# Performance work log

Hardware: AMD Instinct MI355X
Metric: run time of the kernel (lower is better)

## Reference

```python
import jax, jax.numpy as jnp
import numpy as np

N_NODES = 500_000
N_EDGES = 16_000_000


def setup_inputs() -> dict:
    key = jax.random.key(0)
    ks = jax.random.split(key, 8)
    x = jax.random.normal(ks[0], (N_NODES, 6), dtype=jnp.float32)
    edge_index = jax.random.randint(ks[1], (2, N_EDGES), 0, N_NODES, dtype=jnp.int64)
    conv_w = jax.random.normal(ks[2], (4, 6), dtype=jnp.float32) * 0.4
    conv_b = jax.random.normal(ks[3], (4,), dtype=jnp.float32) * 0.1
    fc1_w = jax.random.normal(ks[4], (64, 4), dtype=jnp.float32) * 0.5
    fc1_b = jax.random.normal(ks[5], (64,), dtype=jnp.float32) * 0.1
    fc3_w = jax.random.normal(ks[6], (10, 64), dtype=jnp.float32) * 0.125
    fc3_b = jax.random.normal(ks[7], (10,), dtype=jnp.float32) * 0.1
    return {"x": x, "edge_index": edge_index, "conv_w": conv_w, "conv_b": conv_b,
            "fc1_w": fc1_w, "fc1_b": fc1_b, "fc3_w": fc3_w, "fc3_b": fc3_b}


def reference(x, edge_index, conv_w, conv_b, fc1_w, fc1_b, fc3_w, fc3_b):
    n = x.shape[0]
    loop = jnp.arange(n, dtype=edge_index.dtype)
    # PyG GCNConv default: add self-loops, symmetric normalization
    row = jnp.concatenate([edge_index[0], loop])  # source
    col = jnp.concatenate([edge_index[1], loop])  # target (aggregation index)
    deg = jax.ops.segment_sum(jnp.ones_like(col, dtype=x.dtype), col, num_segments=n)
    dinv = jnp.where(deg > 0, deg ** -0.5, 0.0).astype(x.dtype)
    norm = dinv[row] * dinv[col]                  # [E+N]
    h = x @ conv_w.T                              # [N, 4]
    msg = h[row] * norm[:, None]                  # gather + scale
    agg = jax.ops.segment_sum(msg, col, num_segments=n) + conv_b  # scatter-add
    t = jnp.tanh(agg)
    # F.dropout treated as identity (deterministic eval reference)
    g = jnp.mean(t, axis=0, keepdims=True)        # global_mean_pool, batch=None -> [1, 4]
    hdn = jax.nn.relu(g @ fc1_w.T + fc1_b)
    out = hdn @ fc3_w.T + fc3_b                   # [1, output_size]
    return out
```

## Files before the change

kernel.cpp:

```cpp
#include <hip/hip_runtime.h>
#include <hip/hip_fp16.h>
#include <math.h>


constexpr int NP = 1024;
constexpr int SHIFT = 10;
constexpr unsigned MASK = 1023;
constexpr int NPART_MAX = 512;
constexpr int EPB = 8192;
constexpr int BINB = 512;
constexpr int BT = 512;

struct alignas(8) Half4 { __half2 a, b; };


__global__ __launch_bounds__(BINB) void k_bin(const int* __restrict__ row,
                                              const int* __restrict__ col, int E,
                                              int P, int cap, int* __restrict__ cursor,
                                              unsigned* __restrict__ binned) {
    __shared__ unsigned lbuf[EPB];
    __shared__ int lcount[NPART_MAX];
    __shared__ int lbase[NPART_MAX];
    __shared__ int gbase[NPART_MAX];
    __shared__ int lpos[NPART_MAX];
    __shared__ int sc[NPART_MAX];

    int t = threadIdx.x;
    int start = blockIdx.x * EPB;
    int end = min(start + EPB, E);
    bool full = (end - start) == EPB;

    lcount[t] = 0; lpos[t] = 0;
    __syncthreads();

    if (full) {
        const int4* c4 = (const int4*)(col + start);
#pragma unroll
        for (int i = 0; i < EPB / 4 / BINB; ++i) {
            int4 c = c4[t + i * BINB];
            atomicAdd(&lcount[c.x >> SHIFT], 1);
            atomicAdd(&lcount[c.y >> SHIFT], 1);
            atomicAdd(&lcount[c.z >> SHIFT], 1);
            atomicAdd(&lcount[c.w >> SHIFT], 1);
        }
    } else {
        for (int e = start + t; e < end; e += BINB)
            atomicAdd(&lcount[col[e] >> SHIFT], 1);
    }
    __syncthreads();

    sc[t] = lcount[t];
    __syncthreads();
    for (int off = 1; off < NPART_MAX; off <<= 1) {
        int v = (t >= off) ? sc[t - off] : 0;
        __syncthreads();
        sc[t] += v;
        __syncthreads();
    }
    lbase[t] = sc[t] - lcount[t];
    if (t < P) {
        int c = lcount[t];
        gbase[t] = (c > 0) ? atomicAdd(&cursor[t], c) : 0;
    }
    __syncthreads();

    if (full) {
        const int4* c4 = (const int4*)(col + start);
        const int4* r4 = (const int4*)(row + start);
#pragma unroll
        for (int i = 0; i < EPB / 4 / BINB; ++i) {
            int4 c = c4[t + i * BINB];
            int4 r = r4[t + i * BINB];
            int part, slot;
            part = c.x >> SHIFT; slot = atomicAdd(&lpos[part], 1);
            lbuf[lbase[part] + slot] = ((unsigned)r.x << SHIFT) | ((unsigned)c.x & MASK);
            part = c.y >> SHIFT; slot = atomicAdd(&lpos[part], 1);
            lbuf[lbase[part] + slot] = ((unsigned)r.y << SHIFT) | ((unsigned)c.y & MASK);
            part = c.z >> SHIFT; slot = atomicAdd(&lpos[part], 1);
            lbuf[lbase[part] + slot] = ((unsigned)r.z << SHIFT) | ((unsigned)c.z & MASK);
            part = c.w >> SHIFT; slot = atomicAdd(&lpos[part], 1);
            lbuf[lbase[part] + slot] = ((unsigned)r.w << SHIFT) | ((unsigned)c.w & MASK);
        }
    } else {
        for (int e = start + t; e < end; e += BINB) {
            int r = row[e], c = col[e];
            int part = c >> SHIFT;
            int slot = atomicAdd(&lpos[part], 1);
            lbuf[lbase[part] + slot] = ((unsigned)r << SHIFT) | ((unsigned)c & MASK);
        }
    }
    __syncthreads();

    int lane = t & 63;
    int wave = t >> 6;
    const int nwaves = BINB / 64;
    for (int part = wave; part < P; part += nwaves) {
        int cnt = lcount[part];
        if (cnt == 0) continue;
        int lb = lbase[part];
        int gb = gbase[part];
        unsigned* dst = binned + (size_t)part * cap;
        for (int j = lane; j < cnt; j += 64) {
            int slot = gb + j;
            if (slot < cap) dst[slot] = lbuf[lb + j];
        }
    }
}

__global__ __launch_bounds__(BT) void k_part_node(const unsigned* __restrict__ binned,
                                                  const int* __restrict__ cursor, int cap,
                                                  const float* __restrict__ x,
                                                  const float* __restrict__ conv_w, int n,
                                                  Half4* __restrict__ ph,
                                                  float* __restrict__ dinvg) {
    __shared__ int degs[NP];
    __shared__ float w[24];
    int part = blockIdx.x;
    int tid = threadIdx.x;
    if (tid < 24) w[tid] = conv_w[tid];
    for (int i = tid; i < NP; i += BT) degs[i] = 0;
    __syncthreads();
    int cnt = min(cursor[part], cap);
    const unsigned* bin = binned + (size_t)part * cap;
    const uint4* bin4 = (const uint4*)bin;
    int cnt4 = cnt >> 2;
    for (int i = tid; i < cnt4; i += BT) {
        uint4 v = bin4[i];
        atomicAdd(&degs[v.x & MASK], 1);
        atomicAdd(&degs[v.y & MASK], 1);
        atomicAdd(&degs[v.z & MASK], 1);
        atomicAdd(&degs[v.w & MASK], 1);
    }
    for (int e = (cnt4 << 2) + tid; e < cnt; e += BT)
        atomicAdd(&degs[bin[e] & MASK], 1);
    __syncthreads();
    int base = part * NP;
    for (int i = tid; i < NP; i += BT) {
        int node = base + i;
        if (node >= n) continue;
        float dinv = rsqrtf((float)(degs[i] + 1));
        const float* xr = x + (size_t)node * 6;
        float2 a = *(const float2*)xr;
        float2 b = *(const float2*)(xr + 2);
        float2 cc = *(const float2*)(xr + 4);
        float xv[6] = {a.x, a.y, b.x, b.y, cc.x, cc.y};
        float h0 = 0.f, h1 = 0.f, h2 = 0.f, h3 = 0.f;
#pragma unroll
        for (int j = 0; j < 6; ++j) {
            h0 += xv[j] * w[j];
            h1 += xv[j] * w[6 + j];
            h2 += xv[j] * w[12 + j];
            h3 += xv[j] * w[18 + j];
        }
        Half4 o;
        o.a = __floats2half2_rn(h0 * dinv, h1 * dinv);
        o.b = __floats2half2_rn(h2 * dinv, h3 * dinv);
        ph[node] = o;
        dinvg[node] = dinv;
    }
}

__global__ __launch_bounds__(BT) void k_acc(const unsigned* __restrict__ binned,
                                            const int* __restrict__ cursor, int cap,
                                            const Half4* __restrict__ ph,
                                            const float* __restrict__ dinvg,
                                            const float* __restrict__ conv_b, int n,
                                            float* __restrict__ gsum) {
    __shared__ float S[NP * 5];
    __shared__ float4 red[BT / 64];
    int part = blockIdx.x;
    int tid = threadIdx.x;
    for (int i = tid; i < NP * 5; i += BT) S[i] = 0.f;
    __syncthreads();
    int cnt = min(cursor[part], cap);
    const unsigned* bin = binned + (size_t)part * cap;
    const uint4* bin4 = (const uint4*)bin;
    int cnt4 = cnt >> 2;
    for (int i = tid; i < cnt4; i += BT) {
        uint4 v = bin4[i];
        Half4 h0 = ph[v.x >> SHIFT];
        Half4 h1 = ph[v.y >> SHIFT];
        Half4 h2 = ph[v.z >> SHIFT];
        Half4 h3 = ph[v.w >> SHIFT];
        float2 a, b; float* s;
        a = __half22float2(h0.a); b = __half22float2(h0.b); s = &S[(v.x & MASK) * 5];
        atomicAdd(s + 0, a.x); atomicAdd(s + 1, a.y); atomicAdd(s + 2, b.x); atomicAdd(s + 3, b.y);
        a = __half22float2(h1.a); b = __half22float2(h1.b); s = &S[(v.y & MASK) * 5];
        atomicAdd(s + 0, a.x); atomicAdd(s + 1, a.y); atomicAdd(s + 2, b.x); atomicAdd(s + 3, b.y);
        a = __half22float2(h2.a); b = __half22float2(h2.b); s = &S[(v.z & MASK) * 5];
        atomicAdd(s + 0, a.x); atomicAdd(s + 1, a.y); atomicAdd(s + 2, b.x); atomicAdd(s + 3, b.y);
        a = __half22float2(h3.a); b = __half22float2(h3.b); s = &S[(v.w & MASK) * 5];
        atomicAdd(s + 0, a.x); atomicAdd(s + 1, a.y); atomicAdd(s + 2, b.x); atomicAdd(s + 3, b.y);
    }
    for (int e = (cnt4 << 2) + tid; e < cnt; e += BT) {
        unsigned v = bin[e];
        Half4 h = ph[v >> SHIFT];
        float2 a = __half22float2(h.a), b = __half22float2(h.b);
        float* s = &S[(v & MASK) * 5];
        atomicAdd(s + 0, a.x); atomicAdd(s + 1, a.y); atomicAdd(s + 2, b.x); atomicAdd(s + 3, b.y);
    }
    __syncthreads();
    float b0 = conv_b[0], b1 = conv_b[1], b2 = conv_b[2], b3 = conv_b[3];
    float4 acc = {0.f, 0.f, 0.f, 0.f};
    int base = part * NP;
    for (int i = tid; i < NP; i += BT) {
        int node = base + i;
        if (node >= n) continue;
        float di = dinvg[node];
        Half4 hp = ph[node];
        float2 pa = __half22float2(hp.a), pb = __half22float2(hp.b);
        acc.x += tanhf(di * (S[i * 5 + 0] + pa.x) + b0);
        acc.y += tanhf(di * (S[i * 5 + 1] + pa.y) + b1);
        acc.z += tanhf(di * (S[i * 5 + 2] + pb.x) + b2);
        acc.w += tanhf(di * (S[i * 5 + 3] + pb.y) + b3);
    }
#pragma unroll
    for (int off = 32; off > 0; off >>= 1) {
        acc.x += __shfl_down(acc.x, off);
        acc.y += __shfl_down(acc.y, off);
        acc.z += __shfl_down(acc.z, off);
        acc.w += __shfl_down(acc.w, off);
    }
    int lane = tid & 63, wv = tid >> 6;
    if (lane == 0) red[wv] = acc;
    __syncthreads();
    if (tid == 0) {
        float4 tt = red[0];
        for (int k = 1; k < BT / 64; ++k) {
            tt.x += red[k].x; tt.y += red[k].y; tt.z += red[k].z; tt.w += red[k].w;
        }
        unsafeAtomicAdd(&gsum[0], tt.x);
        unsafeAtomicAdd(&gsum[1], tt.y);
        unsafeAtomicAdd(&gsum[2], tt.z);
        unsafeAtomicAdd(&gsum[3], tt.w);
    }
}

__global__ void k_head(const float* __restrict__ gsum,
                       const float* __restrict__ fc1w, const float* __restrict__ fc1b,
                       const float* __restrict__ fc3w, const float* __restrict__ fc3b,
                       float* __restrict__ out, int n) {
    __shared__ float hdn[64];
    int t = threadIdx.x;
    float g[4];
    float inv_n = 1.0f / (float)n;
#pragma unroll
    for (int j = 0; j < 4; ++j) g[j] = gsum[j] * inv_n;
    if (t < 64) {
        float a = fc1b[t];
#pragma unroll
        for (int j = 0; j < 4; ++j) a += g[j] * fc1w[t * 4 + j];
        hdn[t] = fmaxf(a, 0.f);
    }
    __syncthreads();
    if (t < 10) {
        float a = fc3b[t];
#pragma unroll
        for (int k = 0; k < 64; ++k) a += hdn[k] * fc3w[t * 64 + k];
        out[t] = a;
    }
}


__global__ void k_deg(const int* __restrict__ col, int n_edges, int* __restrict__ deg) {
    int t = blockIdx.x * blockDim.x + threadIdx.x;
    int base = t * 4;
    if (base + 4 <= n_edges) {
        int4 c = *(const int4*)(col + base);
        atomicAdd(&deg[c.x], 1); atomicAdd(&deg[c.y], 1);
        atomicAdd(&deg[c.z], 1); atomicAdd(&deg[c.w], 1);
    } else {
        for (int e = base; e < n_edges; ++e) atomicAdd(&deg[col[e]], 1);
    }
}

__global__ void k_node(const float* __restrict__ x, const float* __restrict__ conv_w,
                       const int* __restrict__ deg, float4* __restrict__ p, int n) {
    int i = blockIdx.x * blockDim.x + threadIdx.x;
    if (i >= n) return;
    const float* xr = x + (size_t)i * 6;
    float2 a = *(const float2*)xr;
    float2 b = *(const float2*)(xr + 2);
    float2 c = *(const float2*)(xr + 4);
    float xv[6] = {a.x, a.y, b.x, b.y, c.x, c.y};
    float dinv = rsqrtf((float)(deg[i] + 1));
    float h0 = 0.f, h1 = 0.f, h2 = 0.f, h3 = 0.f;
#pragma unroll
    for (int j = 0; j < 6; ++j) {
        h0 += xv[j] * conv_w[j];
        h1 += xv[j] * conv_w[6 + j];
        h2 += xv[j] * conv_w[12 + j];
        h3 += xv[j] * conv_w[18 + j];
    }
    float4 o; o.x = h0 * dinv; o.y = h1 * dinv; o.z = h2 * dinv; o.w = h3 * dinv;
    p[i] = o;
}

__global__ void k_scatter(const int* __restrict__ row, const int* __restrict__ col, int n_edges,
                          const float4* __restrict__ p, float* __restrict__ S) {
    int t = blockIdx.x * blockDim.x + threadIdx.x;
    int base = t * 2;
    if (base + 2 <= n_edges) {
        int2 r = *(const int2*)(row + base);
        int2 c = *(const int2*)(col + base);
        float4 p0 = p[r.x], p1 = p[r.y];
        float* s0 = S + 4 * c.x;
        unsafeAtomicAdd(s0 + 0, p0.x); unsafeAtomicAdd(s0 + 1, p0.y);
        unsafeAtomicAdd(s0 + 2, p0.z); unsafeAtomicAdd(s0 + 3, p0.w);
        float* s1 = S + 4 * c.y;
        unsafeAtomicAdd(s1 + 0, p1.x); unsafeAtomicAdd(s1 + 1, p1.y);
        unsafeAtomicAdd(s1 + 2, p1.z); unsafeAtomicAdd(s1 + 3, p1.w);
    } else {
        for (int e = base; e < n_edges; ++e) {
            int r = row[e], c = col[e];
            float4 pv = p[r];
            float* s = S + 4 * c;
            unsafeAtomicAdd(s + 0, pv.x); unsafeAtomicAdd(s + 1, pv.y);
            unsafeAtomicAdd(s + 2, pv.z); unsafeAtomicAdd(s + 3, pv.w);
        }
    }
}

__global__ void k_reduce(const float4* __restrict__ S4, const float4* __restrict__ p,
                         const int* __restrict__ deg, const float* __restrict__ conv_b,
                         int n, float* __restrict__ gsum) {
    int i = blockIdx.x * blockDim.x + threadIdx.x;
    float4 v = {0.f, 0.f, 0.f, 0.f};
    if (i < n) {
        float dinv = rsqrtf((float)(deg[i] + 1));
        float4 s = S4[i];
        float4 pp = p[i];
        v.x = tanhf(dinv * (s.x + pp.x) + conv_b[0]);
        v.y = tanhf(dinv * (s.y + pp.y) + conv_b[1]);
        v.z = tanhf(dinv * (s.z + pp.z) + conv_b[2]);
        v.w = tanhf(dinv * (s.w + pp.w) + conv_b[3]);
    }
#pragma unroll
    for (int off = 32; off > 0; off >>= 1) {
        v.x += __shfl_down(v.x, off);
        v.y += __shfl_down(v.y, off);
        v.z += __shfl_down(v.z, off);
        v.w += __shfl_down(v.w, off);
    }
    __shared__ float4 lds[4];
    int lane = threadIdx.x & 63, w = threadIdx.x >> 6;
    if (lane == 0) lds[w] = v;
    __syncthreads();
    if (threadIdx.x == 0) {
        float4 tt = lds[0];
        for (int k = 1; k < 4; ++k) {
            tt.x += lds[k].x; tt.y += lds[k].y; tt.z += lds[k].z; tt.w += lds[k].w;
        }
        unsafeAtomicAdd(&gsum[0], tt.x); unsafeAtomicAdd(&gsum[1], tt.y);
        unsafeAtomicAdd(&gsum[2], tt.z); unsafeAtomicAdd(&gsum[3], tt.w);
    }
}


extern "C" void kernel_launch(void* const* d_in, const int* in_sizes, int n_in,
                              void* d_out, int out_size, void* d_ws, size_t ws_size,
                              hipStream_t stream) {
    const float* x      = (const float*)d_in[0];
    const int*   ei     = (const int*)d_in[1];
    const float* conv_w = (const float*)d_in[2];
    const float* conv_b = (const float*)d_in[3];
    const float* fc1w   = (const float*)d_in[4];
    const float* fc1b   = (const float*)d_in[5];
    const float* fc3w   = (const float*)d_in[6];
    const float* fc3b   = (const float*)d_in[7];

    int n = in_sizes[0] / 6;
    int E = in_sizes[1] / 2;
    const int* row = ei;
    const int* col = ei + E;

    int P = (n + NP - 1) / NP;
    int avg = (E + P - 1) / P;
    int cap = ((avg + avg / 8 + 2048) + 15) & ~15;

    size_t off = 0;
    size_t cursor_off = off;          off += (size_t)P * sizeof(int);
    off = (off + 15) & ~(size_t)15;
    size_t gsum_off = off;            off += 4 * sizeof(float);
    size_t zero_end = off;
    off = (off + 15) & ~(size_t)15;
    size_t dinv_off = off;            off += (size_t)n * sizeof(float);
    off = (off + 15) & ~(size_t)15;
    size_t ph_off = off;              off += (size_t)n * sizeof(Half4);
    off = (off + 15) & ~(size_t)15;
    size_t bin_off = off;             off += (size_t)P * cap * sizeof(unsigned);
    size_t need = off;

    char* ws = (char*)d_ws;
    bool use_bin = (ws_size >= need) && (P <= NPART_MAX) && (n < (1 << 22));

    if (use_bin) {
        int* cursor = (int*)(ws + cursor_off);
        float* gsum = (float*)(ws + gsum_off);
        float* dinvg = (float*)(ws + dinv_off);
        Half4* ph = (Half4*)(ws + ph_off);
        unsigned* binned = (unsigned*)(ws + bin_off);

        hipMemsetAsync(d_ws, 0, zero_end, stream);
        int bin_blocks = (E + EPB - 1) / EPB;
        k_bin<<<bin_blocks, BINB, 0, stream>>>(row, col, E, P, cap, cursor, binned);
        k_part_node<<<P, BT, 0, stream>>>(binned, cursor, cap, x, conv_w, n, ph, dinvg);
        k_acc<<<P, BT, 0, stream>>>(binned, cursor, cap, ph, dinvg, conv_b, n, gsum);
        k_head<<<1, 64, 0, stream>>>(gsum, fc1w, fc1b, fc3w, fc3b, (float*)d_out, n);
    } else {
        size_t o = 0;
        int* deg = (int*)(ws + o);      o += (size_t)n * sizeof(int);
        o = (o + 15) & ~(size_t)15;
        float* S = (float*)(ws + o);    o += (size_t)n * 4 * sizeof(float);
        float* gsum = (float*)(ws + o);
        size_t zend = o + 4 * sizeof(float);
        o = (zend + 15) & ~(size_t)15;
        float4* p = (float4*)(ws + o);

        hipMemsetAsync(d_ws, 0, zend, stream);
        int t1 = (E + 3) / 4;
        k_deg<<<(t1 + 255) / 256, 256, 0, stream>>>(col, E, deg);
        k_node<<<(n + 255) / 256, 256, 0, stream>>>(x, conv_w, deg, p, n);
        int t3 = (E + 1) / 2;
        k_scatter<<<(t3 + 255) / 256, 256, 0, stream>>>(row, col, E, p, S);
        k_reduce<<<(n + 255) / 256, 256, 0, stream>>>((const float4*)S, p, deg, conv_b, n, gsum);
        k_head<<<1, 64, 0, stream>>>(gsum, fc1w, fc1b, fc3w, fc3b, (float*)d_out, n);
    }
}
```

Before: 624.3 us.

## Split per-partition degree and accumulate work across multiple blocks with global merge

Each partition's binned edges are now processed by SPLIT blocks instead of one. The per-partition degree pass and the accumulate pass each merge their shared-memory partials into global arrays with atomics. The node transform and the final tanh/mean reduction move into separate grid-wide kernels. Nontemporal loads and stores are used for streaming binned data and edge rows, and the bin capacity slack is reduced. This targets low occupancy from only about 489 blocks per pass, at the cost of extra kernels, global atomics, a larger memset, and a risk of bin overflow with the tighter cap.

```diff
diff --git a/kernel.cpp b/kernel.cpp
--- a/kernel.cpp
+++ b/kernel.cpp
@@ -10,8 +10,13 @@
 constexpr int EPB = 8192;
 constexpr int BINB = 512;
 constexpr int BT = 512;
+constexpr int SPLIT = 4;
 
 struct alignas(8) Half4 { __half2 a, b; };
+
+typedef unsigned u32x4 __attribute__((ext_vector_type(4)));
+typedef int      i32x4 __attribute__((ext_vector_type(4)));
+typedef float    f32x4 __attribute__((ext_vector_type(4)));
 
 
 __global__ __launch_bounds__(BINB) void k_bin(const int* __restrict__ row,
@@ -66,11 +71,11 @@
 
     if (full) {
         const int4* c4 = (const int4*)(col + start);
-        const int4* r4 = (const int4*)(row + start);
+        const i32x4* r4 = (const i32x4*)(row + start);
 #pragma unroll
         for (int i = 0; i < EPB / 4 / BINB; ++i) {
             int4 c = c4[t + i * BINB];
-            int4 r = r4[t + i * BINB];
+            i32x4 r = __builtin_nontemporal_load(&r4[t + i * BINB]);
             int part, slot;
             part = c.x >> SHIFT; slot = atomicAdd(&lpos[part], 1);
             lbuf[lbase[part] + slot] = ((unsigned)r.x << SHIFT) | ((unsigned)c.x & MASK);
@@ -102,82 +107,88 @@
         unsigned* dst = binned + (size_t)part * cap;
         for (int j = lane; j < cnt; j += 64) {
             int slot = gb + j;
-            if (slot < cap) dst[slot] = lbuf[lb + j];
-        }
-    }
-}
-
-__global__ __launch_bounds__(BT) void k_part_node(const unsigned* __restrict__ binned,
-                                                  const int* __restrict__ cursor, int cap,
-                                                  const float* __restrict__ x,
-                                                  const float* __restrict__ conv_w, int n,
-                                                  Half4* __restrict__ ph,
-                                                  float* __restrict__ dinvg) {
+            if (slot < cap) __builtin_nontemporal_store(lbuf[lb + j], &dst[slot]);
+        }
+    }
+}
+
+__global__ __launch_bounds__(BT) void k_deg_bin(const unsigned* __restrict__ binned,
+                                                const int* __restrict__ cursor, int cap,
+                                                int n, int* __restrict__ deg) {
     __shared__ int degs[NP];
-    __shared__ float w[24];
-    int part = blockIdx.x;
+    int part = blockIdx.x / SPLIT;
+    int sub = blockIdx.x - part * SPLIT;
     int tid = threadIdx.x;
-    if (tid < 24) w[tid] = conv_w[tid];
     for (int i = tid; i < NP; i += BT) degs[i] = 0;
     __syncthreads();
     int cnt = min(cursor[part], cap);
     const unsigned* bin = binned + (size_t)part * cap;
-    const uint4* bin4 = (const uint4*)bin;
+    const u32x4* bin4 = (const u32x4*)bin;
     int cnt4 = cnt >> 2;
-    for (int i = tid; i < cnt4; i += BT) {
-        uint4 v = bin4[i];
+    for (int i = tid + sub * BT; i < cnt4; i += BT * SPLIT) {
+        u32x4 v = __builtin_nontemporal_load(&bin4[i]);
         atomicAdd(&degs[v.x & MASK], 1);
         atomicAdd(&degs[v.y & MASK], 1);
         atomicAdd(&degs[v.z & MASK], 1);
         atomicAdd(&degs[v.w & MASK], 1);
     }
-    for (int e = (cnt4 << 2) + tid; e < cnt; e += BT)
-        atomicAdd(&degs[bin[e] & MASK], 1);
+    if (sub == 0) {
+        for (int e = (cnt4 << 2) + tid; e < cnt; e += BT)
+            atomicAdd(&degs[bin[e] & MASK], 1);
+    }
     __syncthreads();
     int base = part * NP;
     for (int i = tid; i < NP; i += BT) {
         int node = base + i;
-        if (node >= n) continue;
-        float dinv = rsqrtf((float)(degs[i] + 1));
-        const float* xr = x + (size_t)node * 6;
-        float2 a = *(const float2*)xr;
-        float2 b = *(const float2*)(xr + 2);
-        float2 cc = *(const float2*)(xr + 4);
-        float xv[6] = {a.x, a.y, b.x, b.y, cc.x, cc.y};
-        float h0 = 0.f, h1 = 0.f, h2 = 0.f, h3 = 0.f;
-#pragma unroll
-        for (int j = 0; j < 6; ++j) {
-            h0 += xv[j] * w[j];
-            h1 += xv[j] * w[6 + j];
-            h2 += xv[j] * w[12 + j];
-            h3 += xv[j] * w[18 + j];
-        }
-        Half4 o;
-        o.a = __floats2half2_rn(h0 * dinv, h1 * dinv);
-        o.b = __floats2half2_rn(h2 * dinv, h3 * dinv);
-        ph[node] = o;
-        dinvg[node] = dinv;
-    }
-}
-
-__global__ __launch_bounds__(BT) void k_acc(const unsigned* __restrict__ binned,
-                                            const int* __restrict__ cursor, int cap,
-                                            const Half4* __restrict__ ph,
-                                            const float* __restrict__ dinvg,
-                                            const float* __restrict__ conv_b, int n,
-                                            float* __restrict__ gsum) {
+        if (node < n && degs[i] > 0) atomicAdd(&deg[node], degs[i]);
+    }
+}
+
+__global__ __launch_bounds__(256) void k_node2(const float* __restrict__ x,
+                                               const float* __restrict__ conv_w,
+                                               const int* __restrict__ deg, int n,
+                                               Half4* __restrict__ ph) {
+    __shared__ float w[24];
+    if (threadIdx.x < 24) w[threadIdx.x] = conv_w[threadIdx.x];
+    __syncthreads();
+    int i = blockIdx.x * 256 + threadIdx.x;
+    if (i >= n) return;
+    float dinv = rsqrtf((float)(deg[i] + 1));
+    const float* xr = x + (size_t)i * 6;
+    float2 a = *(const float2*)xr;
+    float2 b = *(const float2*)(xr + 2);
+    float2 cc = *(const float2*)(xr + 4);
+    float xv[6] = {a.x, a.y, b.x, b.y, cc.x, cc.y};
+    float h0 = 0.f, h1 = 0.f, h2 = 0.f, h3 = 0.f;
+#pragma unroll
+    for (int j = 0; j < 6; ++j) {
+        h0 += xv[j] * w[j];
+        h1 += xv[j] * w[6 + j];
+        h2 += xv[j] * w[12 + j];
+        h3 += xv[j] * w[18 + j];
+    }
+    Half4 o;
+    o.a = __floats2half2_rn(h0 * dinv, h1 * dinv);
+    o.b = __floats2half2_rn(h2 * dinv, h3 * dinv);
+    ph[i] = o;
+}
+
+__global__ __launch_bounds__(BT) void k_acc2(const unsigned* __restrict__ binned,
+                                             const int* __restrict__ cursor, int cap,
+                                             const Half4* __restrict__ ph,
+                                             float* __restrict__ Sg) {
     __shared__ float S[NP * 5];
-    __shared__ float4 red[BT / 64];
-    int part = blockIdx.x;
+    int part = blockIdx.x / SPLIT;
+    int sub = blockIdx.x - part * SPLIT;
     int tid = threadIdx.x;
     for (int i = tid; i < NP * 5; i += BT) S[i] = 0.f;
     __syncthreads();
     int cnt = min(cursor[part], cap);
     const unsigned* bin = binned + (size_t)part * cap;
-    const uint4* bin4 = (const uint4*)bin;
+    const u32x4* bin4 = (const u32x4*)bin;
     int cnt4 = cnt >> 2;
-    for (int i = tid; i < cnt4; i += BT) {
-        uint4 v = bin4[i];
+    for (int i = tid + sub * BT; i < cnt4; i += BT * SPLIT) {
+        u32x4 v = __builtin_nontemporal_load(&bin4[i]);
         Half4 h0 = ph[v.x >> SHIFT];
         Half4 h1 = ph[v.y >> SHIFT];
         Half4 h2 = ph[v.z >> SHIFT];
@@ -192,41 +203,53 @@
         a = __half22float2(h3.a); b = __half22float2(h3.b); s = &S[(v.w & MASK) * 5];
         atomicAdd(s + 0, a.x); atomicAdd(s + 1, a.y); atomicAdd(s + 2, b.x); atomicAdd(s + 3, b.y);
     }
-    for (int e = (cnt4 << 2) + tid; e < cnt; e += BT) {
-        unsigned v = bin[e];
-        Half4 h = ph[v >> SHIFT];
-        float2 a = __half22float2(h.a), b = __half22float2(h.b);
-        float* s = &S[(v & MASK) * 5];
-        atomicAdd(s + 0, a.x); atomicAdd(s + 1, a.y); atomicAdd(s + 2, b.x); atomicAdd(s + 3, b.y);
-    }
-    __syncthreads();
-    float b0 = conv_b[0], b1 = conv_b[1], b2 = conv_b[2], b3 = conv_b[3];
-    float4 acc = {0.f, 0.f, 0.f, 0.f};
-    int base = part * NP;
-    for (int i = tid; i < NP; i += BT) {
-        int node = base + i;
-        if (node >= n) continue;
-        float di = dinvg[node];
-        Half4 hp = ph[node];
+    if (sub == 0) {
+        for (int e = (cnt4 << 2) + tid; e < cnt; e += BT) {
+            unsigned v = bin[e];
+            Half4 h = ph[v >> SHIFT];
+            float2 a = __half22float2(h.a), b = __half22float2(h.b);
+            float* s = &S[(v & MASK) * 5];
+            atomicAdd(s + 0, a.x); atomicAdd(s + 1, a.y); atomicAdd(s + 2, b.x); atomicAdd(s + 3, b.y);
+        }
+    }
+    __syncthreads();
+    float* dst = Sg + (size_t)part * NP * 4;
+    for (int i = tid; i < NP * 4; i += BT) {
+        unsafeAtomicAdd(&dst[i], S[(i >> 2) * 5 + (i & 3)]);
+    }
+}
+
+__global__ __launch_bounds__(256) void k_finish(const float* __restrict__ Sg,
+                                                const Half4* __restrict__ ph,
+                                                const int* __restrict__ deg,
+                                                const float* __restrict__ conv_b, int n,
+                                                float* __restrict__ gsum) {
+    int i = blockIdx.x * 256 + threadIdx.x;
+    float4 v = {0.f, 0.f, 0.f, 0.f};
+    if (i < n) {
+        float dinv = rsqrtf((float)(deg[i] + 1));
+        f32x4 s = __builtin_nontemporal_load((const f32x4*)Sg + i);
+        Half4 hp = ph[i];
         float2 pa = __half22float2(hp.a), pb = __half22float2(hp.b);
-        acc.x += tanhf(di * (S[i * 5 + 0] + pa.x) + b0);
-        acc.y += tanhf(di * (S[i * 5 + 1] + pa.y) + b1);
-        acc.z += tanhf(di * (S[i * 5 + 2] + pb.x) + b2);
-        acc.w += tanhf(di * (S[i * 5 + 3] + pb.y) + b3);
+        v.x = tanhf(dinv * (s.x + pa.x) + conv_b[0]);
+        v.y = tanhf(dinv * (s.y + pa.y) + conv_b[1]);
+        v.z = tanhf(dinv * (s.z + pb.x) + conv_b[2]);
+        v.w = tanhf(dinv * (s.w + pb.y) + conv_b[3]);
     }
 #pragma unroll
     for (int off = 32; off > 0; off >>= 1) {
-        acc.x += __shfl_down(acc.x, off);
-        acc.y += __shfl_down(acc.y, off);
-        acc.z += __shfl_down(acc.z, off);
-        acc.w += __shfl_down(acc.w, off);
-    }
-    int lane = tid & 63, wv = tid >> 6;
-    if (lane == 0) red[wv] = acc;
-    __syncthreads();
-    if (tid == 0) {
+        v.x += __shfl_down(v.x, off);
+        v.y += __shfl_down(v.y, off);
+        v.z += __shfl_down(v.z, off);
+        v.w += __shfl_down(v.w, off);
+    }
+    __shared__ float4 red[4];
+    int lane = threadIdx.x & 63, w = threadIdx.x >> 6;
+    if (lane == 0) red[w] = v;
+    __syncthreads();
+    if (threadIdx.x == 0) {
         float4 tt = red[0];
-        for (int k = 1; k < BT / 64; ++k) {
+        for (int k = 1; k < 4; ++k) {
             tt.x += red[k].x; tt.y += red[k].y; tt.z += red[k].z; tt.w += red[k].w;
         }
         unsafeAtomicAdd(&gsum[0], tt.x);
@@ -376,15 +399,17 @@
 
     int P = (n + NP - 1) / NP;
     int avg = (E + P - 1) / P;
-    int cap = ((avg + avg / 8 + 2048) + 15) & ~15;
+    int cap = ((avg + avg / 32 + 1024) + 15) & ~15;
 
     size_t off = 0;
     size_t cursor_off = off;          off += (size_t)P * sizeof(int);
     off = (off + 15) & ~(size_t)15;
     size_t gsum_off = off;            off += 4 * sizeof(float);
+    off = (off + 15) & ~(size_t)15;
+    size_t deg_off = off;             off += (size_t)n * sizeof(int);
+    off = (off + 15) & ~(size_t)15;
+    size_t S_off = off;               off += (size_t)P * NP * 4 * sizeof(float);
     size_t zero_end = off;
-    off = (off + 15) & ~(size_t)15;
-    size_t dinv_off = off;            off += (size_t)n * sizeof(float);
     off = (off + 15) & ~(size_t)15;
     size_t ph_off = off;              off += (size_t)n * sizeof(Half4);
     off = (off + 15) & ~(size_t)15;
@@ -397,15 +422,18 @@
     if (use_bin) {
         int* cursor = (int*)(ws + cursor_off);
         float* gsum = (float*)(ws + gsum_off);
-        float* dinvg = (float*)(ws + dinv_off);
+        int* deg = (int*)(ws + deg_off);
+        float* Sg = (float*)(ws + S_off);
         Half4* ph = (Half4*)(ws + ph_off);
         unsigned* binned = (unsigned*)(ws + bin_off);
 
         hipMemsetAsync(d_ws, 0, zero_end, stream);
         int bin_blocks = (E + EPB - 1) / EPB;
         k_bin<<<bin_blocks, BINB, 0, stream>>>(row, col, E, P, cap, cursor, binned);
-        k_part_node<<<P, BT, 0, stream>>>(binned, cursor, cap, x, conv_w, n, ph, dinvg);
-        k_acc<<<P, BT, 0, stream>>>(binned, cursor, cap, ph, dinvg, conv_b, n, gsum);
+        k_deg_bin<<<P * SPLIT, BT, 0, stream>>>(binned, cursor, cap, n, deg);
+        k_node2<<<(n + 255) / 256, 256, 0, stream>>>(x, conv_w, deg, n, ph);
+        k_acc2<<<P * SPLIT, BT, 0, stream>>>(binned, cursor, cap, ph, Sg);
+        k_finish<<<(n + 255) / 256, 256, 0, stream>>>(Sg, ph, deg, conv_b, n, gsum);
         k_head<<<1, 64, 0, stream>>>(gsum, fc1w, fc1b, fc3w, fc3b, (float*)d_out, n);
     } else {
         size_t o = 0;
```

Measured after the change: 751.2 us. +20.3%, slower.

## Split degree counting across blocks and add nontemporal loads/stores for bins

Applied to the files above, without the earlier changes.

Replaces the per-partition degree+node kernel with a degree kernel that splits each partition across SPLIT blocks and merges counts into a global degree array with atomics, then a separate flat node kernel computes dinv and the projected features. Bin reads and writes use nontemporal builtins to avoid polluting cache, and the bin capacity slack is reduced. This raises parallelism in the degree pass at the cost of an extra kernel launch, a global degree array to zero, and global atomics.

```diff
diff --git a/kernel.cpp b/kernel.cpp
--- a/kernel.cpp
+++ b/kernel.cpp
@@ -10,8 +10,13 @@
 constexpr int EPB = 8192;
 constexpr int BINB = 512;
 constexpr int BT = 512;
+constexpr int SPLIT = 4;
 
 struct alignas(8) Half4 { __half2 a, b; };
+
+typedef unsigned u32x4 __attribute__((ext_vector_type(4)));
+typedef int      i32x4 __attribute__((ext_vector_type(4)));
+typedef float    f32x4 __attribute__((ext_vector_type(4)));
 
 
 __global__ __launch_bounds__(BINB) void k_bin(const int* __restrict__ row,
@@ -66,11 +71,11 @@
 
     if (full) {
         const int4* c4 = (const int4*)(col + start);
-        const int4* r4 = (const int4*)(row + start);
+        const i32x4* r4 = (const i32x4*)(row + start);
 #pragma unroll
         for (int i = 0; i < EPB / 4 / BINB; ++i) {
             int4 c = c4[t + i * BINB];
-            int4 r = r4[t + i * BINB];
+            i32x4 r = __builtin_nontemporal_load(&r4[t + i * BINB]);
             int part, slot;
             part = c.x >> SHIFT; slot = atomicAdd(&lpos[part], 1);
             lbuf[lbase[part] + slot] = ((unsigned)r.x << SHIFT) | ((unsigned)c.x & MASK);
@@ -102,62 +107,72 @@
         unsigned* dst = binned + (size_t)part * cap;
         for (int j = lane; j < cnt; j += 64) {
             int slot = gb + j;
-            if (slot < cap) dst[slot] = lbuf[lb + j];
-        }
-    }
-}
-
-__global__ __launch_bounds__(BT) void k_part_node(const unsigned* __restrict__ binned,
-                                                  const int* __restrict__ cursor, int cap,
-                                                  const float* __restrict__ x,
-                                                  const float* __restrict__ conv_w, int n,
-                                                  Half4* __restrict__ ph,
-                                                  float* __restrict__ dinvg) {
+            if (slot < cap) __builtin_nontemporal_store(lbuf[lb + j], &dst[slot]);
+        }
+    }
+}
+
+__global__ __launch_bounds__(BT) void k_deg_bin(const unsigned* __restrict__ binned,
+                                                const int* __restrict__ cursor, int cap,
+                                                int n, int* __restrict__ deg) {
     __shared__ int degs[NP];
-    __shared__ float w[24];
-    int part = blockIdx.x;
+    int part = blockIdx.x / SPLIT;
+    int sub = blockIdx.x - part * SPLIT;
     int tid = threadIdx.x;
-    if (tid < 24) w[tid] = conv_w[tid];
     for (int i = tid; i < NP; i += BT) degs[i] = 0;
     __syncthreads();
     int cnt = min(cursor[part], cap);
     const unsigned* bin = binned + (size_t)part * cap;
-    const uint4* bin4 = (const uint4*)bin;
+    const u32x4* bin4 = (const u32x4*)bin;
     int cnt4 = cnt >> 2;
-    for (int i = tid; i < cnt4; i += BT) {
-        uint4 v = bin4[i];
+    for (int i = tid + sub * BT; i < cnt4; i += BT * SPLIT) {
+        u32x4 v = __builtin_nontemporal_load(&bin4[i]);
         atomicAdd(&degs[v.x & MASK], 1);
         atomicAdd(&degs[v.y & MASK], 1);
         atomicAdd(&degs[v.z & MASK], 1);
         atomicAdd(&degs[v.w & MASK], 1);
     }
-    for (int e = (cnt4 << 2) + tid; e < cnt; e += BT)
-        atomicAdd(&degs[bin[e] & MASK], 1);
+    if (sub == 0) {
+        for (int e = (cnt4 << 2) + tid; e < cnt; e += BT)
+            atomicAdd(&degs[bin[e] & MASK], 1);
+    }
     __syncthreads();
     int base = part * NP;
     for (int i = tid; i < NP; i += BT) {
         int node = base + i;
-        if (node >= n) continue;
-        float dinv = rsqrtf((float)(degs[i] + 1));
-        const float* xr = x + (size_t)node * 6;
-        float2 a = *(const float2*)xr;
-        float2 b = *(const float2*)(xr + 2);
-        float2 cc = *(const float2*)(xr + 4);
-        float xv[6] = {a.x, a.y, b.x, b.y, cc.x, cc.y};
-        float h0 = 0.f, h1 = 0.f, h2 = 0.f, h3 = 0.f;
-#pragma unroll
-        for (int j = 0; j < 6; ++j) {
-            h0 += xv[j] * w[j];
-            h1 += xv[j] * w[6 + j];
-            h2 += xv[j] * w[12 + j];
-            h3 += xv[j] * w[18 + j];
-        }
-        Half4 o;
-        o.a = __floats2half2_rn(h0 * dinv, h1 * dinv);
-        o.b = __floats2half2_rn(h2 * dinv, h3 * dinv);
-        ph[node] = o;
-        dinvg[node] = dinv;
-    }
+        if (node < n && degs[i] > 0) atomicAdd(&deg[node], degs[i]);
+    }
+}
+
+__global__ __launch_bounds__(256) void k_node2(const float* __restrict__ x,
+                                               const float* __restrict__ conv_w,
+                                               const int* __restrict__ deg, int n,
+                                               Half4* __restrict__ ph,
+                                               float* __restrict__ dinvg) {
+    __shared__ float w[24];
+    if (threadIdx.x < 24) w[threadIdx.x] = conv_w[threadIdx.x];
+    __syncthreads();
+    int i = blockIdx.x * 256 + threadIdx.x;
+    if (i >= n) return;
+    float dinv = rsqrtf((float)(deg[i] + 1));
+    const float* xr = x + (size_t)i * 6;
+    float2 a = *(const float2*)xr;
+    float2 b = *(const float2*)(xr + 2);
+    float2 cc = *(const float2*)(xr + 4);
+    float xv[6] = {a.x, a.y, b.x, b.y, cc.x, cc.y};
+    float h0 = 0.f, h1 = 0.f, h2 = 0.f, h3 = 0.f;
+#pragma unroll
+    for (int j = 0; j < 6; ++j) {
+        h0 += xv[j] * w[j];
+        h1 += xv[j] * w[6 + j];
+        h2 += xv[j] * w[12 + j];
+        h3 += xv[j] * w[18 + j];
+    }
+    Half4 o;
+    o.a = __floats2half2_rn(h0 * dinv, h1 * dinv);
+    o.b = __floats2half2_rn(h2 * dinv, h3 * dinv);
+    ph[i] = o;
+    dinvg[i] = dinv;
 }
 
 __global__ __launch_bounds__(BT) void k_acc(const unsigned* __restrict__ binned,
@@ -174,10 +189,10 @@
     __syncthreads();
     int cnt = min(cursor[part], cap);
     const unsigned* bin = binned + (size_t)part * cap;
-    const uint4* bin4 = (const uint4*)bin;
+    const u32x4* bin4 = (const u32x4*)bin;
     int cnt4 = cnt >> 2;
     for (int i = tid; i < cnt4; i += BT) {
-        uint4 v = bin4[i];
+        u32x4 v = __builtin_nontemporal_load(&bin4[i]);
         Half4 h0 = ph[v.x >> SHIFT];
         Half4 h1 = ph[v.y >> SHIFT];
         Half4 h2 = ph[v.z >> SHIFT];
@@ -376,12 +391,14 @@
 
     int P = (n + NP - 1) / NP;
     int avg = (E + P - 1) / P;
-    int cap = ((avg + avg / 8 + 2048) + 15) & ~15;
+    int cap = ((avg + avg / 32 + 1024) + 15) & ~15;
 
     size_t off = 0;
     size_t cursor_off = off;          off += (size_t)P * sizeof(int);
     off = (off + 15) & ~(size_t)15;
     size_t gsum_off = off;            off += 4 * sizeof(float);
+    off = (off + 15) & ~(size_t)15;
+    size_t deg_off = off;             off += (size_t)n * sizeof(int);
     size_t zero_end = off;
     off = (off + 15) & ~(size_t)15;
     size_t dinv_off = off;            off += (size_t)n * sizeof(float);
@@ -392,11 +409,12 @@
     size_t need = off;
 
     char* ws = (char*)d_ws;
-    bool use_bin = (ws_size >= need) && (P <= NPART_MAX) && (n < (1 << 22));
+    bool use_bin = (ws_size >= need) && (P <= NPART_MAX) && (n < (1 << 21));
 
     if (use_bin) {
         int* cursor = (int*)(ws + cursor_off);
         float* gsum = (float*)(ws + gsum_off);
+        int* deg = (int*)(ws + deg_off);
         float* dinvg = (float*)(ws + dinv_off);
         Half4* ph = (Half4*)(ws + ph_off);
         unsigned* binned = (unsigned*)(ws + bin_off);
@@ -404,7 +422,8 @@
         hipMemsetAsync(d_ws, 0, zero_end, stream);
         int bin_blocks = (E + EPB - 1) / EPB;
         k_bin<<<bin_blocks, BINB, 0, stream>>>(row, col, E, P, cap, cursor, binned);
-        k_part_node<<<P, BT, 0, stream>>>(binned, cursor, cap, x, conv_w, n, ph, dinvg);
+        k_deg_bin<<<P * SPLIT, BT, 0, stream>>>(binned, cursor, cap, n, deg);
+        k_node2<<<(n + 255) / 256, 256, 0, stream>>>(x, conv_w, deg, n, ph, dinvg);
         k_acc<<<P, BT, 0, stream>>>(binned, cursor, cap, ph, dinvg, conv_b, n, gsum);
         k_head<<<1, 64, 0, stream>>>(gsum, fc1w, fc1b, fc3w, fc3b, (float*)d_out, n);
     } else {
```

After: 645.2 us. 3.4% more time.
